# Kernel optimization log

Measured on AMD Instinct MI355X. Metric: run time of the kernel, lower is better.

Reference implementation:

```python
import jax, jax.numpy as jnp
import numpy as np

B, S, H, E, V, NSTEPS = 8, 128, 512, 512, 32000, 8


def setup_inputs() -> dict:
    key = jax.random.key(0)
    ks = jax.random.split(key, 24)

    def lin(k, fi, fo):
        return (jax.random.normal(k, (fi, fo), jnp.float32) / np.sqrt(fi).astype(np.float32))

    return {
        "input_ids": jax.random.randint(ks[0], (B, S), 0, V),
        "tree_ids": jax.random.randint(ks[1], (B, NSTEPS, 3, S), 0, S),
        "emb": jax.random.normal(ks[2], (V, E), jnp.float32) * 0.02,
        "W_ioux": lin(ks[3], E, 3 * H),
        "W_iouh_r": lin(ks[4], H, 3 * H),
        "b_iouh_r": jnp.zeros((3 * H,), jnp.float32),
        "W_iouh_l": lin(ks[5], H, 3 * H),
        "b_iouh_l": jnp.zeros((3 * H,), jnp.float32),
        "W_fx": lin(ks[6], E, H),
        "W_fh0": lin(ks[7], H, H),
        "b_fh0": jnp.zeros((H,), jnp.float32),
        "W_fh1": lin(ks[8], H, H),
        "b_fh1": jnp.zeros((H,), jnp.float32),
        "W_fh2": lin(ks[9], H, H),
        "b_fh2": jnp.zeros((H,), jnp.float32),
        "W_fh3": lin(ks[10], H, H),
        "b_fh3": jnp.zeros((H,), jnp.float32),
    }


def _scatter_rows(vals, idx):
    # out[b, idx[b, j], k] += vals[b, j, k]  (torch scatter_add_ along dim 1)
    return jax.vmap(lambda v, i: jnp.zeros_like(v).at[i].add(v))(vals, idx)


def _gather_rows(vals, idx):
    # out[b, j, k] = vals[b, idx[b, j], k]  (torch gather along dim 1)
    return jnp.take_along_axis(vals, idx[:, :, None], axis=1)


def _masked_scatter(dest, mask_rows, src):
    # Exact torch masked_scatter_ semantics: flatten mask/src, fill True slots
    # with consecutive elements of flattened src.
    m = jnp.broadcast_to(mask_rows[:, :, None], dest.shape).reshape(-1)
    pos = jnp.clip(jnp.cumsum(m) - 1, 0, None)
    out = jnp.where(m, src.reshape(-1)[pos], dest.reshape(-1))
    return out.reshape(dest.shape)


def reference(input_ids, tree_ids, emb, W_ioux, W_iouh_r, b_iouh_r, W_iouh_l,
              b_iouh_l, W_fx, W_fh0, b_fh0, W_fh1, b_fh1, W_fh2, b_fh2,
              W_fh3, b_fh3):
    x = emb[input_ids]                      # [B, S, E]
    Hs = W_fx.shape[1]
    iou_x = x @ W_ioux                      # [B, S, 3H], loop-invariant
    fx_x = x @ W_fx                         # [B, S, H],  loop-invariant
    h0 = jnp.zeros(x.shape[:2] + (Hs,), x.dtype)
    c0 = jnp.zeros_like(h0)
    steps = jnp.transpose(tree_ids, (1, 0, 2, 3))  # [n_steps, B, 3, S]

    def step(carry, t):
        h, c = carry
        idx_d, idx_r, idx_l = t[:, 0], t[:, 1], t[:, 2]
        iou_hr = h @ W_iouh_r + b_iouh_r
        iou_hl = h @ W_iouh_l + b_iouh_l
        # torch scatter_add_ with an index of width H into a 3H buffer only
        # touches the first H channels -- replicate that exactly.
        scat = _scatter_rows(iou_hr[..., :Hs], idx_r) + _scatter_rows(iou_hl[..., :Hs], idx_l)
        iou = iou_x.at[..., :Hs].add(scat)
        i, o, u = jnp.split(iou, 3, axis=-1)
        i, o, u = jax.nn.sigmoid(i), jax.nn.sigmoid(o), jnp.tanh(u)
        # fh0 and fh1 share idx_r, fh2 and fh3 share idx_l -> fold linearly.
        fh_r = h @ (W_fh0 + W_fh1) + (b_fh0 + b_fh1)
        fh_l = h @ (W_fh2 + W_fh3) + (b_fh2 + b_fh3)
        f = jax.nn.sigmoid(_gather_rows(fx_x, idx_d)
                           + _gather_rows(fh_r, idx_r)
                           + _gather_rows(fh_l, idx_l))
        fc = f * c
        c_full = i * u + _scatter_rows(fc, idx_d)
        h_full = o * jnp.tanh(c_full)
        mask = idx_d != 0
        h_new = _masked_scatter(h, mask, h_full)
        c_new = _masked_scatter(c, mask, c_full)
        return (h_new, c_new), None

    (h, c), _ = jax.lax.scan(step, (h0, c0), steps)
    return h
```

## Files before the change

### kernel.cpp

```cpp
#include <hip/hip_runtime.h>
#include <hip/hip_bf16.h>

#define B_ 8
#define S_ 128
#define H_ 512
#define E_ 512
#define NST 8
#define R_ 1024
#define N2 2048
#define KD 512
#define LDA 72
#define NBLK 512
#define GRP 64

typedef __hip_bfloat16 bf16;
typedef __attribute__((ext_vector_type(8))) short v8s;
typedef __attribute__((ext_vector_type(4))) float v4f;
typedef unsigned long long u64;

__device__ __forceinline__ float sigm(float x){ return 1.0f/(1.0f + expf(-x)); }
__device__ __forceinline__ float load_in(const void* p, long long i, int isb){
    return isb ? __bfloat162float(((const bf16*)p)[i]) : ((const float*)p)[i];
}
__device__ __forceinline__ int idx_read(const int* p, int j, int is64){
    return is64 ? p[2*j] : p[j];
}
__device__ __forceinline__ unsigned short f2b(float v){
    bf16 b = __float2bfloat16(v);
    return *(unsigned short*)&b;
}

__device__ __forceinline__ float vload1f(const float* p){
    return __hip_atomic_load(p, __ATOMIC_RELAXED, __HIP_MEMORY_SCOPE_AGENT);
}
__device__ __forceinline__ void vstore1(float* p, float v){
    __hip_atomic_store(p, v, __ATOMIC_RELAXED, __HIP_MEMORY_SCOPE_AGENT);
}
__device__ __forceinline__ void vstore_hb2(unsigned short* p, unsigned short a, unsigned short b){
    unsigned int u = (unsigned)a | ((unsigned)b << 16);
    __hip_atomic_store((unsigned int*)p, u, __ATOMIC_RELAXED, __HIP_MEMORY_SCOPE_AGENT);
}
__device__ __forceinline__ v8s vload16(const unsigned short* p){
    union { u64 u[2]; v8s v; } c;
    c.u[0] = __hip_atomic_load((const u64*)p,     __ATOMIC_RELAXED, __HIP_MEMORY_SCOPE_AGENT);
    c.u[1] = __hip_atomic_load(((const u64*)p)+1, __ATOMIC_RELAXED, __HIP_MEMORY_SCOPE_AGENT);
    return c.v;
}

__device__ __forceinline__ void gsync(int* bar, int gen){
    __syncthreads();
    if (threadIdx.x == 0){
        int g = blockIdx.x >> 6;
        int* ga = bar + 64*(1+g);
        int* gd = bar + 64*(9+g);
        int old = __hip_atomic_fetch_add(ga, 1, __ATOMIC_RELAXED, __HIP_MEMORY_SCOPE_AGENT);
        if (old + 1 == GRP*gen){
            __hip_atomic_fetch_add(bar, GRP, __ATOMIC_RELAXED, __HIP_MEMORY_SCOPE_AGENT);
            while (__hip_atomic_load(bar, __ATOMIC_RELAXED, __HIP_MEMORY_SCOPE_AGENT) < NBLK*gen)
                __builtin_amdgcn_s_sleep(2);
            __hip_atomic_fetch_add(gd, 1, __ATOMIC_RELAXED, __HIP_MEMORY_SCOPE_AGENT);
        } else {
            while (__hip_atomic_load(gd, __ATOMIC_RELAXED, __HIP_MEMORY_SCOPE_AGENT) < gen)
                __builtin_amdgcn_s_sleep(2);
        }
    }
    __syncthreads();
}

__global__ void probe_all(const void* t0, const void* t1, const void* t2, const void* t3,
                          const void* t4, const void* t5, const void* t6, const void* t7,
                          const void* t8, const void* t9, const void* t10, const void* t11,
                          const void* t12, const void* t13, const void* t14,
                          const int* __restrict__ ids, const int* __restrict__ tree,
                          int* __restrict__ flags){
    const void* ts[15] = {t0,t1,t2,t3,t4,t5,t6,t7,t8,t9,t10,t11,t12,t13,t14};
    int bid = blockIdx.x, t = threadIdx.x;
    int bad = 0;
    if (bid < 15){
        if (t < 512){
            unsigned short u = ((const unsigned short*)ts[bid])[t];
            bad = (((u >> 7) & 0xFF) >= 140);
        }
    } else {
        const int* p = (bid == 15) ? ids : tree;
        int n = (bid == 15) ? 1024 : 2048;
        for (int j = t; j < n; j += 1024)
            if (j & 1) bad |= (p[j] != 0);
    }
    unsigned long long bl = __ballot(bad);
    __shared__ int acc[16];
    if ((t & 63) == 0) acc[t >> 6] = (bl != 0ull) ? 1 : 0;
    __syncthreads();
    if (t == 0){
        int any = 0;
        for (int w = 0; w < 16; ++w) any |= acc[w];
        flags[(bid < 15) ? bid : (16 + bid - 15)] = any ? 0 : 1;
    }
}

#define NB2 320
#define GS2 (NB2*512)
__global__ __launch_bounds__(512)
void rank_pack(const void* __restrict__ Wioux, const void* __restrict__ Wfx,
               const void* __restrict__ Wr, const void* __restrict__ Wl,
               const void* __restrict__ W0, const void* __restrict__ W1,
               const void* __restrict__ W2, const void* __restrict__ W3,
               const void* __restrict__ br, const void* __restrict__ bl,
               const void* __restrict__ b0, const void* __restrict__ b1,
               const void* __restrict__ b2, const void* __restrict__ b3,
               const int* __restrict__ ids, const void* __restrict__ emb,
               const int* __restrict__ tree,
               unsigned short* __restrict__ WxT, unsigned short* __restrict__ WcatT,
               float* __restrict__ bcat, unsigned short* __restrict__ xb,
               float* __restrict__ h0,
               int* __restrict__ msk, int* __restrict__ rnk, int* __restrict__ cnt,
               const int* __restrict__ flags, int* __restrict__ bar){
    int bid = blockIdx.x, tid = threadIdx.x;
    int is64 = flags[17];
    if (bid == 0){
        for (int i = tid; i < 64*81; i += 512) bar[i] = 0;
    }
    if (bid < 8){
        int st = bid;
        for (int c = tid; c < R_; c += 512){
            cnt[(0*NST + st)*R_ + c] = 0;
            cnt[(1*NST + st)*R_ + c] = 0;
            cnt[(2*NST + st)*R_ + c] = 0;
        }
        __syncthreads();
        __shared__ int wt[8];
        int runbase = 0;
        for (int ch = 0; ch < 2; ++ch){
            int t = ch*512 + tid;
            int b = t >> 7, s = t & 127;
            int base = (b*NST + st)*3*S_;
            int d0 = idx_read(tree, base + s, is64);
            int rd = (b<<7) + d0;
            int rr = (b<<7) + idx_read(tree, base + S_ + s, is64);
            int rl = (b<<7) + idx_read(tree, base + 2*S_ + s, is64);
            int m = (d0 != 0) ? 1 : 0;
            unsigned long long bal = __ballot(m);
            int lane = tid & 63, wv = tid >> 6;
            if (lane == 0) wt[wv] = __popcll(bal);
            __syncthreads();
            int bp = runbase, tot = 0;
            for (int w = 0; w < wv; ++w) bp += wt[w];
            for (int w = 0; w < 8; ++w) tot += wt[w];
            int rank = bp + __popcll(bal & ((1ull << lane) - 1ull));
            msk[st*R_ + t] = m;
            rnk[st*R_ + t] = m ? rank : 0;
            atomicAdd(&cnt[(0*NST + st)*R_ + rr], 1);
            atomicAdd(&cnt[(1*NST + st)*R_ + rl], 1);
            atomicAdd(&cnt[(2*NST + st)*R_ + rd], 1);
            runbase += tot;
            __syncthreads();
        }
    }
    int gt = bid*512 + tid;
    {
        int f_wx = flags[1], f_wf = flags[6];
        for (int u = gt; u < 131072; u += GS2){
            int n = u >> 6, k0 = (u & 63)*8;
            unsigned short tmp[8];
            #pragma unroll
            for (int i = 0; i < 8; ++i){
                float v = (n < 1536) ? load_in(Wioux, (long long)(k0+i)*1536 + n, f_wx)
                                     : load_in(Wfx,   (long long)(k0+i)*512 + (n-1536), f_wf);
                tmp[i] = f2b(v);
            }
            *(v8s*)&WxT[(size_t)n*KD + k0] = *(v8s*)tmp;
        }
    }
    {
        int fWr=flags[2], fWl=flags[4], fW0=flags[7], fW1=flags[9], fW2=flags[11], fW3=flags[13];
        for (int u = gt; u < 131072; u += GS2){
            int n = u >> 6, k0 = (u & 63)*8;
            unsigned short tmp[8];
            #pragma unroll
            for (int i = 0; i < 8; ++i){
                long long k = k0 + i;
                float v;
                if      (n <  512) v = load_in(Wr, k*1536 + n, fWr);
                else if (n < 1024) v = load_in(Wl, k*1536 + (n-512), fWl);
                else if (n < 1536) { int c = n-1024; v = load_in(W0, k*512+c, fW0) + load_in(W1, k*512+c, fW1); }
                else               { int c = n-1536; v = load_in(W2, k*512+c, fW2) + load_in(W3, k*512+c, fW3); }
                tmp[i] = f2b(v);
            }
            *(v8s*)&WcatT[(size_t)n*KD + k0] = *(v8s*)tmp;
        }
    }
    {
        int fbr=flags[3], fbl=flags[5], fb0=flags[8], fb1=flags[10], fb2=flags[12], fb3=flags[14];
        for (int n = gt; n < 2048; n += GS2){
            float v;
            if      (n <  512) v = load_in(br, n, fbr);
            else if (n < 1024) v = load_in(bl, n-512, fbl);
            else if (n < 1536) v = load_in(b0, n-1024, fb0) + load_in(b1, n-1024, fb1);
            else               v = load_in(b2, n-1536, fb2) + load_in(b3, n-1536, fb3);
            bcat[n] = v;
        }
    }
    {
        int f_emb = flags[0], i64i = flags[16];
        for (int u = gt; u < 65536; u += GS2){
            int r = u >> 6, c0 = (u & 63)*8;
            long long base = (long long)idx_read(ids, r, i64i)*E_ + c0;
            unsigned short tmp[8];
            #pragma unroll
            for (int i = 0; i < 8; ++i) tmp[i] = f2b(load_in(emb, base + i, f_emb));
            *(v8s*)&xb[(size_t)r*KD + c0] = *(v8s*)tmp;
        }
    }
    for (int u = gt; u < 262144; u += GS2)
        ((float4*)h0)[u] = make_float4(0.f,0.f,0.f,0.f);
}

__global__ void csr_scan(const int* __restrict__ cnt, int* __restrict__ off,
                         int* __restrict__ cur){
    int st = blockIdx.x, a = blockIdx.y;
    int t = threadIdx.x;
    int base = (a*NST + st)*R_;
    __shared__ int sh[R_];
    int v = cnt[base + t];
    sh[t] = v;
    __syncthreads();
    for (int d = 1; d < R_; d <<= 1){
        int x = (t >= d) ? sh[t - d] : 0;
        __syncthreads();
        sh[t] += x;
        __syncthreads();
    }
    int excl = sh[t] - v;
    off[base + t] = excl;
    cur[base + t] = excl;
}

__global__ __launch_bounds__(512)
void csr_fill(const int* __restrict__ tree, int* __restrict__ cur,
              int* __restrict__ ent, const int* __restrict__ flags){
    int is64 = flags[17];
    int st = blockIdx.x;
    for (int ch = 0; ch < 2; ++ch){
        int t = ch*512 + threadIdx.x;
        int b = t >> 7, s = t & 127;
        int base = (b*NST + st)*3*S_;
        int rd = (b<<7) + idx_read(tree, base + s, is64);
        int rr = (b<<7) + idx_read(tree, base + S_ + s, is64);
        int rl = (b<<7) + idx_read(tree, base + 2*S_ + s, is64);
        int p0 = atomicAdd(&cur[(0*NST + st)*R_ + rr], 1);
        ent[(0*NST + st)*R_ + p0] = t;
        int p1 = atomicAdd(&cur[(1*NST + st)*R_ + rl], 1);
        ent[(1*NST + st)*R_ + p1] = t;
        int p2 = atomicAdd(&cur[(2*NST + st)*R_ + rd], 1);
        ent[(2*NST + st)*R_ + p2] = t | (rr << 10) | (rl << 20);
    }
}

__device__ __forceinline__ void gemm_phase(const unsigned short* __restrict__ A,
               const unsigned short* __restrict__ BT,
               const float* __restrict__ bias,
               float* __restrict__ C,
               short* __restrict__ SMEM)
{
    int bid = blockIdx.x;
    int bn = (bid & 7)*4 + ((bid >> 3) & 3);
    int bm = bid >> 5;
    int tid = threadIdx.x;
    int lane = tid & 63, wave = tid >> 6;
    int grp = wave >> 2, w4 = wave & 3;
    int wm = w4 & 1, wn = w4 >> 1;
    int lm = lane & 15, quad = lane >> 4;
    short* As = SMEM + grp*(2*64*LDA);
    short* Bs = As + 64*LDA;
    v4f acc[2][2];
    #pragma unroll
    for (int i=0;i<2;++i)
        #pragma unroll
        for (int j=0;j<2;++j) acc[i][j] = (v4f)0.0f;

    int t = tid & 255;
    int srow = t >> 3, sg = (t & 7)*8;
    int kb = grp*256;
    const unsigned short* Ab = A  + (size_t)(bm*64)*KD + kb;
    const unsigned short* Bb = BT + (size_t)(bn*64)*KD + kb;
    v8s pa[4][2], pb[2];
    #pragma unroll
    for (int q=0;q<4;++q)
        #pragma unroll
        for (int j=0;j<2;++j)
            pa[q][j] = vload16(Ab + (size_t)(j*32+srow)*KD + q*64 + sg);
    #pragma unroll
    for (int j=0;j<2;++j)
        pb[j] = *(const v8s*)(Bb + (size_t)(j*32+srow)*KD + sg);
    #pragma unroll
    for (int q = 0; q < 4; ++q){
        #pragma unroll
        for (int j=0;j<2;++j){
            *(v8s*)&As[(j*32+srow)*LDA + sg] = pa[q][j];
            *(v8s*)&Bs[(j*32+srow)*LDA + sg] = pb[j];
        }
        __syncthreads();
        if (q < 3){
            #pragma unroll
            for (int j=0;j<2;++j)
                pb[j] = *(const v8s*)(Bb + (size_t)(j*32+srow)*KD + (q+1)*64 + sg);
        }
        #pragma unroll
        for (int kk = 0; kk < 64; kk += 32){
            v8s af[2], bf[2];
            #pragma unroll
            for (int i=0;i<2;++i){
                af[i] = *(const v8s*)&As[(wm*32 + i*16 + lm)*LDA + kk + quad*8];
                bf[i] = *(const v8s*)&Bs[(wn*32 + i*16 + lm)*LDA + kk + quad*8];
            }
            #pragma unroll
            for (int i=0;i<2;++i)
                #pragma unroll
                for (int j=0;j<2;++j)
                    acc[i][j] = __builtin_amdgcn_mfma_f32_16x16x32_bf16(af[i], bf[j], acc[i][j], 0, 0, 0);
        }
        __syncthreads();
    }
    float* Red = (float*)SMEM;
    if (grp){
        #pragma unroll
        for (int i=0;i<2;++i)
            #pragma unroll
            for (int j=0;j<2;++j)
                #pragma unroll
                for (int rg=0;rg<4;++rg)
                    Red[(wm*32 + i*16 + quad*4 + rg)*64 + (wn*32 + j*16 + lm)] = acc[i][j][rg];
    }
    __syncthreads();
    if (!grp){
        #pragma unroll
        for (int j=0;j<2;++j){
            int n = bn*64 + wn*32 + j*16 + lm;
            float bv = bias ? bias[n] : 0.0f;
            #pragma unroll
            for (int i=0;i<2;++i){
                int m0 = bm*64 + wm*32 + i*16 + quad*4;
                #pragma unroll
                for (int rg = 0; rg < 4; ++rg){
                    float v = acc[i][j][rg] + Red[(wm*32 + i*16 + quad*4 + rg)*64 + (wn*32 + j*16 + lm)] + bv;
                    vstore1(&C[(size_t)(m0+rg)*N2 + n], v);
                }
            }
        }
    }
}

__device__ __forceinline__ void epi_phase(const float* __restrict__ XO,
              const float* __restrict__ T, int tstr,
              const float* __restrict__ hc, const float* __restrict__ cc,
              float* __restrict__ hn, float* __restrict__ cn,
              unsigned short* __restrict__ hb, float* __restrict__ out,
              const int* __restrict__ msk, const int* __restrict__ rnk,
              const int* __restrict__ cnt, const int* __restrict__ off,
              const int* __restrict__ ent, int st, int last, int r0)
{
    int c = threadIdx.x;
    #pragma unroll
    for (int rr2 = 0; rr2 < 2; ++rr2){
        int r = r0 + rr2;
        if (!msk[st*R_ + r]){
            float hv = vload1f(&hc[(size_t)r*H_ + c]);
            if (last){
                out[(size_t)r*H_ + c] = hv;
            } else {
                vstore1(&hn[(size_t)r*H_ + c], hv);
                vstore1(&cn[(size_t)r*H_ + c], vload1f(&cc[(size_t)r*H_ + c]));
                unsigned v16 = f2b(hv);
                unsigned o16 = __shfl_down((int)v16, 1);
                if (!(c & 1)) vstore_hb2(&hb[(size_t)r*KD + c], (unsigned short)v16, (unsigned short)o16);
            }
            continue;
        }
        int j = rnk[st*R_ + r];
        int bR = off[(0*NST+st)*R_ + j], dR = cnt[(0*NST+st)*R_ + j];
        int bL = off[(1*NST+st)*R_ + j], dL = cnt[(1*NST+st)*R_ + j];
        int bD = off[(2*NST+st)*R_ + j], dD = cnt[(2*NST+st)*R_ + j];
        const int* eR = ent + (0*NST+st)*R_ + bR;
        const int* eL = ent + (1*NST+st)*R_ + bL;
        const int* eD = ent + (2*NST+st)*R_ + bD;
        const float* xo = XO + (size_t)j*N2;
        float scv = 0.f;
        {
            int e = 0;
            for (; e + 4 <= dR; e += 4){
                int a0=eR[e], a1=eR[e+1], a2=eR[e+2], a3=eR[e+3];
                float t0 = vload1f(&T[(size_t)a0*tstr + c]);
                float t1 = vload1f(&T[(size_t)a1*tstr + c]);
                float t2 = vload1f(&T[(size_t)a2*tstr + c]);
                float t3 = vload1f(&T[(size_t)a3*tstr + c]);
                scv += (t0 + t1) + (t2 + t3);
            }
            for (; e < dR; ++e) scv += vload1f(&T[(size_t)eR[e]*tstr + c]);
        }
        {
            int e = 0;
            for (; e + 4 <= dL; e += 4){
                int a0=eL[e], a1=eL[e+1], a2=eL[e+2], a3=eL[e+3];
                float t0 = vload1f(&T[(size_t)a0*tstr + 512 + c]);
                float t1 = vload1f(&T[(size_t)a1*tstr + 512 + c]);
                float t2 = vload1f(&T[(size_t)a2*tstr + 512 + c]);
                float t3 = vload1f(&T[(size_t)a3*tstr + 512 + c]);
                scv += (t0 + t1) + (t2 + t3);
            }
            for (; e < dL; ++e) scv += vload1f(&T[(size_t)eL[e]*tstr + 512 + c]);
        }
        float fxv = vload1f(&xo[1536 + c]);
        float csc = 0.f;
        {
            int e = 0;
            for (; e + 2 <= dD; e += 2){
                int p0 = eD[e], p1 = eD[e+1];
                int s0 = p0 & 1023, ra0 = (p0 >> 10) & 1023, rb0 = (p0 >> 20) & 1023;
                int s1 = p1 & 1023, ra1 = (p1 >> 10) & 1023, rb1 = (p1 >> 20) & 1023;
                float ta0 = vload1f(&T[(size_t)ra0*tstr + 1024 + c]);
                float tb0 = vload1f(&T[(size_t)rb0*tstr + 1536 + c]);
                float cv0 = vload1f(&cc[(size_t)s0*H_ + c]);
                float ta1 = vload1f(&T[(size_t)ra1*tstr + 1024 + c]);
                float tb1 = vload1f(&T[(size_t)rb1*tstr + 1536 + c]);
                float cv1 = vload1f(&cc[(size_t)s1*H_ + c]);
                csc += sigm(fxv + ta0 + tb0) * cv0 + sigm(fxv + ta1 + tb1) * cv1;
            }
            for (; e < dD; ++e){
                int pk = eD[e];
                int s  = pk & 1023, ra = (pk >> 10) & 1023, rb = (pk >> 20) & 1023;
                float ta = vload1f(&T[(size_t)ra*tstr + 1024 + c]);
                float tb = vload1f(&T[(size_t)rb*tstr + 1536 + c]);
                float cv = vload1f(&cc[(size_t)s*H_ + c]);
                csc += sigm(fxv + ta + tb) * cv;
            }
        }
        float ig = sigm(vload1f(&xo[c]) + scv);
        float og = sigm(vload1f(&xo[512 + c]));
        float ug = tanhf(vload1f(&xo[1024 + c]));
        float cf = ig*ug + csc;
        float hf = og * tanhf(cf);
        if (last){
            out[(size_t)r*H_ + c] = hf;
        } else {
            vstore1(&hn[(size_t)r*H_ + c], hf);
            vstore1(&cn[(size_t)r*H_ + c], cf);
            unsigned v16 = f2b(hf);
            unsigned o16 = __shfl_down((int)v16, 1);
            if (!(c & 1)) vstore_hb2(&hb[(size_t)r*KD + c], (unsigned short)v16, (unsigned short)o16);
        }
    }
}

__global__ __launch_bounds__(512, 4)
void chain_all(const unsigned short* __restrict__ xb,
               const unsigned short* __restrict__ WxT,
               const unsigned short* __restrict__ WcatT,
               const float* __restrict__ bcat,
               float* __restrict__ XO, float* __restrict__ T,
               float* __restrict__ h0, float* __restrict__ c0,
               float* __restrict__ h1, float* __restrict__ c1,
               unsigned short* __restrict__ hb, float* __restrict__ out,
               const int* __restrict__ msk, const int* __restrict__ rnk,
               const int* __restrict__ cnt, const int* __restrict__ off,
               const int* __restrict__ ent, int* bar)
{
    __shared__ short SMEM[4*64*LDA];
    int bid = blockIdx.x;
    int bG  = bid >> 6;
    int r0  = (bG << 7) + ((bid & 63) << 1);
    int* sc = bar + 64*17;
    int gen = 0;

    auto sig = [&](int st){
        __syncthreads();
        if (threadIdx.x == 0)
            __hip_atomic_fetch_add(sc + 64*(st*8 + bG), 1,
                                   __ATOMIC_RELAXED, __HIP_MEMORY_SCOPE_AGENT);
    };
    auto waitc = [&](int st, int b){
        int* p = sc + 64*(st*8 + b);
        while (__hip_atomic_load(p, __ATOMIC_RELAXED, __HIP_MEMORY_SCOPE_AGENT) < 64)
            __builtin_amdgcn_s_sleep(1);
    };

    gemm_phase(xb, WxT, (const float*)nullptr, XO, SMEM);
    sig(0);
    {
        int m0 = msk[r0], m1 = msk[r0 + 1];
        int jb0 = m0 ? (rnk[r0] >> 7) : bG;
        int jb1 = m1 ? (rnk[r0 + 1] >> 7) : bG;
        if (threadIdx.x == 0){
            waitc(0, jb0);
            if (jb1 != jb0) waitc(0, jb1);
        }
        __syncthreads();
        epi_phase(XO, bcat, 0, h0, c0, h1, c1, hb, out,
                  msk, rnk, cnt, off, ent, 0, 0, r0);
    }
    gsync(bar, ++gen);

    for (int st = 1; st < NST; ++st){
        const float* hcp = (st & 1) ? h1 : h0;
        const float* ccp = (st & 1) ? c1 : c0;
        float* hnp = (st & 1) ? h0 : h1;
        float* cnp = (st & 1) ? c0 : c1;
        gemm_phase(hb, WcatT, bcat, T, SMEM);
        sig(st);
        {
            int m0 = msk[st*R_ + r0], m1 = msk[st*R_ + r0 + 1];
            int jb0 = m0 ? (rnk[st*R_ + r0] >> 7) : bG;
            int jb1 = m1 ? (rnk[st*R_ + r0 + 1] >> 7) : bG;
            if (threadIdx.x == 0){
                waitc(st, bG);
                if (jb0 != bG) waitc(st, jb0);
                if (jb1 != bG && jb1 != jb0) waitc(st, jb1);
            }
            __syncthreads();
            epi_phase(XO, T, N2, hcp, ccp, hnp, cnp, hb, out,
                      msk, rnk, cnt, off, ent, st, (st == NST-1) ? 1 : 0, r0);
        }
        if (st < NST-1) gsync(bar, ++gen);
    }
}

extern "C" void kernel_launch(void* const* d_in, const int* in_sizes, int n_in,
                              void* d_out, int out_size, void* d_ws, size_t ws_size,
                              hipStream_t stream) {
    const int* input_ids = (const int*)d_in[0];
    const int* tree      = (const int*)d_in[1];

    char* wp = (char*)d_ws;
    auto alloc = [&](size_t bytes) -> void* {
        void* q = (void*)wp;
        wp += (bytes + 255) & ~(size_t)255;
        return q;
    };
    float*          XO     = (float*)alloc((size_t)R_*N2*4);
    float*          T      = (float*)alloc((size_t)R_*N2*4);
    float*          h0     = (float*)alloc((size_t)R_*H_*4);
    float*          c0     = (float*)alloc((size_t)R_*H_*4);
    float*          h1     = (float*)alloc((size_t)R_*H_*4);
    float*          c1     = (float*)alloc((size_t)R_*H_*4);
    unsigned short* WxT    = (unsigned short*)alloc((size_t)N2*KD*2);
    unsigned short* WcatT  = (unsigned short*)alloc((size_t)N2*KD*2);
    float*          bcat   = (float*)alloc((size_t)N2*4);
    unsigned short* xb     = (unsigned short*)alloc((size_t)R_*KD*2);
    unsigned short* hb     = (unsigned short*)alloc((size_t)R_*KD*2);
    int*            msk    = (int*)alloc((size_t)NST*R_*4);
    int*            rnk    = (int*)alloc((size_t)NST*R_*4);
    int*            cnt    = (int*)alloc((size_t)3*NST*R_*4);
    int*            off    = (int*)alloc((size_t)3*NST*R_*4);
    int*            cur    = (int*)alloc((size_t)3*NST*R_*4);
    int*            ent    = (int*)alloc((size_t)3*NST*R_*4);
    int*            flags  = (int*)alloc(256);
    int*            bar    = (int*)alloc(32768);
    float*          out    = (float*)d_out;

    hipLaunchKernelGGL(probe_all, dim3(17), dim3(1024), 0, stream,
                       d_in[2], d_in[3], d_in[4], d_in[5], d_in[6], d_in[7], d_in[8],
                       d_in[9], d_in[10], d_in[11], d_in[12], d_in[13], d_in[14],
                       d_in[15], d_in[16], input_ids, tree, flags);
    hipLaunchKernelGGL(rank_pack, dim3(NB2), dim3(512), 0, stream,
                       d_in[3], d_in[8],
                       d_in[4], d_in[6], d_in[9], d_in[11], d_in[13], d_in[15],
                       d_in[5], d_in[7], d_in[10], d_in[12], d_in[14], d_in[16],
                       input_ids, d_in[2], tree,
                       WxT, WcatT, bcat, xb, h0, msk, rnk, cnt, flags, bar);
    hipLaunchKernelGGL(csr_scan, dim3(NST, 3), dim3(1024), 0, stream, cnt, off, cur);
    hipLaunchKernelGGL(csr_fill, dim3(NST), dim3(512), 0, stream, tree, cur, ent, flags);

    hipLaunchKernelGGL(chain_all, dim3(NBLK), dim3(512), 0, stream,
                       xb, WxT, WcatT, bcat, XO, T, h0, c0, h1, c1, hb, out,
                       msk, rnk, cnt, off, ent, bar);
}
```

Baseline: 324.6 us.

## Replace atomic loads with plain loads plus per-XCD cache invalidation at barriers

Device-scope relaxed atomic loads on T, XO, h/c and the GEMM A operand are replaced by ordinary cached loads. Visibility across XCDs is kept by having one block per XCD issue a buffer_inv at each grid barrier, while the other blocks on that XCD wait and do a local invalidate. The fine-grained per-group dependency signalling (sig/waitc) is replaced by full grid barriers, adding one extra barrier after the first GEMM. This trades cheaper vectorised cached loads for a more global synchronisation pattern, and relies on the invalidate protocol being sufficient for correctness.

```diff
diff --git a/kernel.cpp b/kernel.cpp
--- a/kernel.cpp
+++ b/kernel.cpp
@@ -30,9 +30,6 @@
     return *(unsigned short*)&b;
 }
 
-__device__ __forceinline__ float vload1f(const float* p){
-    return __hip_atomic_load(p, __ATOMIC_RELAXED, __HIP_MEMORY_SCOPE_AGENT);
-}
 __device__ __forceinline__ void vstore1(float* p, float v){
     __hip_atomic_store(p, v, __ATOMIC_RELAXED, __HIP_MEMORY_SCOPE_AGENT);
 }
@@ -40,14 +37,14 @@
     unsigned int u = (unsigned)a | ((unsigned)b << 16);
     __hip_atomic_store((unsigned int*)p, u, __ATOMIC_RELAXED, __HIP_MEMORY_SCOPE_AGENT);
 }
-__device__ __forceinline__ v8s vload16(const unsigned short* p){
-    union { u64 u[2]; v8s v; } c;
-    c.u[0] = __hip_atomic_load((const u64*)p,     __ATOMIC_RELAXED, __HIP_MEMORY_SCOPE_AGENT);
-    c.u[1] = __hip_atomic_load(((const u64*)p)+1, __ATOMIC_RELAXED, __HIP_MEMORY_SCOPE_AGENT);
-    return c.v;
-}
-
-__device__ __forceinline__ void gsync(int* bar, int gen){
+
+__device__ __forceinline__ int get_xcd(){
+    int x;
+    asm volatile("s_getreg_b32 %0, hwreg(HW_REG_XCC_ID)" : "=s"(x));
+    return x & 7;
+}
+
+__device__ __forceinline__ void gsync(int* bar, int gen, int inv_gen){
     __syncthreads();
     if (threadIdx.x == 0){
         int g = blockIdx.x >> 6;
@@ -62,6 +59,21 @@
         } else {
             while (__hip_atomic_load(gd, __ATOMIC_RELAXED, __HIP_MEMORY_SCOPE_AGENT) < gen)
                 __builtin_amdgcn_s_sleep(2);
+        }
+        if (inv_gen > 0){
+            int x  = get_xcd();
+            int nx = __hip_atomic_load(bar + 64*(17+x), __ATOMIC_RELAXED, __HIP_MEMORY_SCOPE_AGENT);
+            int* xa = bar + 64*(25+x);
+            int* xr = bar + 64*(33+x);
+            int o2 = __hip_atomic_fetch_add(xa, 1, __ATOMIC_RELAXED, __HIP_MEMORY_SCOPE_AGENT);
+            if (o2 + 1 == nx*inv_gen){
+                asm volatile("buffer_inv sc0 sc1\n\ts_waitcnt vmcnt(0)" ::: "memory");
+                __hip_atomic_store(xr, inv_gen, __ATOMIC_RELAXED, __HIP_MEMORY_SCOPE_AGENT);
+            } else {
+                while (__hip_atomic_load(xr, __ATOMIC_RELAXED, __HIP_MEMORY_SCOPE_AGENT) < inv_gen)
+                    __builtin_amdgcn_s_sleep(1);
+                asm volatile("buffer_inv sc0\n\ts_waitcnt vmcnt(0)" ::: "memory");
+            }
         }
     }
     __syncthreads();
@@ -288,7 +300,7 @@
     for (int q=0;q<4;++q)
         #pragma unroll
         for (int j=0;j<2;++j)
-            pa[q][j] = vload16(Ab + (size_t)(j*32+srow)*KD + q*64 + sg);
+            pa[q][j] = *(const v8s*)(Ab + (size_t)(j*32+srow)*KD + q*64 + sg);
     #pragma unroll
     for (int j=0;j<2;++j)
         pb[j] = *(const v8s*)(Bb + (size_t)(j*32+srow)*KD + sg);
@@ -364,12 +376,12 @@
     for (int rr2 = 0; rr2 < 2; ++rr2){
         int r = r0 + rr2;
         if (!msk[st*R_ + r]){
-            float hv = vload1f(&hc[(size_t)r*H_ + c]);
+            float hv = hc[(size_t)r*H_ + c];
             if (last){
                 out[(size_t)r*H_ + c] = hv;
             } else {
                 vstore1(&hn[(size_t)r*H_ + c], hv);
-                vstore1(&cn[(size_t)r*H_ + c], vload1f(&cc[(size_t)r*H_ + c]));
+                vstore1(&cn[(size_t)r*H_ + c], cc[(size_t)r*H_ + c]);
                 unsigned v16 = f2b(hv);
                 unsigned o16 = __shfl_down((int)v16, 1);
                 if (!(c & 1)) vstore_hb2(&hb[(size_t)r*KD + c], (unsigned short)v16, (unsigned short)o16);
@@ -389,27 +401,27 @@
             int e = 0;
             for (; e + 4 <= dR; e += 4){
                 int a0=eR[e], a1=eR[e+1], a2=eR[e+2], a3=eR[e+3];
-                float t0 = vload1f(&T[(size_t)a0*tstr + c]);
-                float t1 = vload1f(&T[(size_t)a1*tstr + c]);
-                float t2 = vload1f(&T[(size_t)a2*tstr + c]);
-                float t3 = vload1f(&T[(size_t)a3*tstr + c]);
+                float t0 = T[(size_t)a0*tstr + c];
+                float t1 = T[(size_t)a1*tstr + c];
+                float t2 = T[(size_t)a2*tstr + c];
+                float t3 = T[(size_t)a3*tstr + c];
                 scv += (t0 + t1) + (t2 + t3);
             }
-            for (; e < dR; ++e) scv += vload1f(&T[(size_t)eR[e]*tstr + c]);
+            for (; e < dR; ++e) scv += T[(size_t)eR[e]*tstr + c];
         }
         {
             int e = 0;
             for (; e + 4 <= dL; e += 4){
                 int a0=eL[e], a1=eL[e+1], a2=eL[e+2], a3=eL[e+3];
-                float t0 = vload1f(&T[(size_t)a0*tstr + 512 + c]);
-                float t1 = vload1f(&T[(size_t)a1*tstr + 512 + c]);
-                float t2 = vload1f(&T[(size_t)a2*tstr + 512 + c]);
-                float t3 = vload1f(&T[(size_t)a3*tstr + 512 + c]);
+                float t0 = T[(size_t)a0*tstr + 512 + c];
+                float t1 = T[(size_t)a1*tstr + 512 + c];
+                float t2 = T[(size_t)a2*tstr + 512 + c];
+                float t3 = T[(size_t)a3*tstr + 512 + c];
                 scv += (t0 + t1) + (t2 + t3);
             }
-            for (; e < dL; ++e) scv += vload1f(&T[(size_t)eL[e]*tstr + 512 + c]);
-        }
-        float fxv = vload1f(&xo[1536 + c]);
+            for (; e < dL; ++e) scv += T[(size_t)eL[e]*tstr + 512 + c];
+        }
+        float fxv = xo[1536 + c];
         float csc = 0.f;
         {
             int e = 0;
@@ -417,26 +429,26 @@
                 int p0 = eD[e], p1 = eD[e+1];
                 int s0 = p0 & 1023, ra0 = (p0 >> 10) & 1023, rb0 = (p0 >> 20) & 1023;
                 int s1 = p1 & 1023, ra1 = (p1 >> 10) & 1023, rb1 = (p1 >> 20) & 1023;
-                float ta0 = vload1f(&T[(size_t)ra0*tstr + 1024 + c]);
-                float tb0 = vload1f(&T[(size_t)rb0*tstr + 1536 + c]);
-                float cv0 = vload1f(&cc[(size_t)s0*H_ + c]);
-                float ta1 = vload1f(&T[(size_t)ra1*tstr + 1024 + c]);
-                float tb1 = vload1f(&T[(size_t)rb1*tstr + 1536 + c]);
-                float cv1 = vload1f(&cc[(size_t)s1*H_ + c]);
+                float ta0 = T[(size_t)ra0*tstr + 1024 + c];
+                float tb0 = T[(size_t)rb0*tstr + 1536 + c];
+                float cv0 = cc[(size_t)s0*H_ + c];
+                float ta1 = T[(size_t)ra1*tstr + 1024 + c];
+                float tb1 = T[(size_t)rb1*tstr + 1536 + c];
+                float cv1 = cc[(size_t)s1*H_ + c];
                 csc += sigm(fxv + ta0 + tb0) * cv0 + sigm(fxv + ta1 + tb1) * cv1;
             }
             for (; e < dD; ++e){
                 int pk = eD[e];
                 int s  = pk & 1023, ra = (pk >> 10) & 1023, rb = (pk >> 20) & 1023;
-                float ta = vload1f(&T[(size_t)ra*tstr + 1024 + c]);
-                float tb = vload1f(&T[(size_t)rb*tstr + 1536 + c]);
-                float cv = vload1f(&cc[(size_t)s*H_ + c]);
+                float ta = T[(size_t)ra*tstr + 1024 + c];
+                float tb = T[(size_t)rb*tstr + 1536 + c];
+                float cv = cc[(size_t)s*H_ + c];
                 csc += sigm(fxv + ta + tb) * cv;
             }
         }
-        float ig = sigm(vload1f(&xo[c]) + scv);
-        float og = sigm(vload1f(&xo[512 + c]));
-        float ug = tanhf(vload1f(&xo[1024 + c]));
+        float ig = sigm(xo[c] + scv);
+        float og = sigm(xo[512 + c]);
+        float ug = tanhf(xo[1024 + c]);
         float cf = ig*ug + csc;
         float hf = og * tanhf(cf);
         if (last){
@@ -465,39 +477,17 @@
                const int* __restrict__ ent, int* bar)
 {
     __shared__ short SMEM[4*64*LDA];
-    int bid = blockIdx.x;
-    int bG  = bid >> 6;
-    int r0  = (bG << 7) + ((bid & 63) << 1);
-    int* sc = bar + 64*17;
-    int gen = 0;
-
-    auto sig = [&](int st){
-        __syncthreads();
-        if (threadIdx.x == 0)
-            __hip_atomic_fetch_add(sc + 64*(st*8 + bG), 1,
-                                   __ATOMIC_RELAXED, __HIP_MEMORY_SCOPE_AGENT);
-    };
-    auto waitc = [&](int st, int b){
-        int* p = sc + 64*(st*8 + b);
-        while (__hip_atomic_load(p, __ATOMIC_RELAXED, __HIP_MEMORY_SCOPE_AGENT) < 64)
-            __builtin_amdgcn_s_sleep(1);
-    };
+    if (threadIdx.x == 0){
+        int x = get_xcd();
+        __hip_atomic_fetch_add(bar + 64*(17+x), 1, __ATOMIC_RELAXED, __HIP_MEMORY_SCOPE_AGENT);
+    }
+    int r0 = blockIdx.x*2;
+    int gen = 0, ig = 0;
 
     gemm_phase(xb, WxT, (const float*)nullptr, XO, SMEM);
-    sig(0);
-    {
-        int m0 = msk[r0], m1 = msk[r0 + 1];
-        int jb0 = m0 ? (rnk[r0] >> 7) : bG;
-        int jb1 = m1 ? (rnk[r0 + 1] >> 7) : bG;
-        if (threadIdx.x == 0){
-            waitc(0, jb0);
-            if (jb1 != jb0) waitc(0, jb1);
-        }
-        __syncthreads();
-        epi_phase(XO, bcat, 0, h0, c0, h1, c1, hb, out,
-                  msk, rnk, cnt, off, ent, 0, 0, r0);
-    }
-    gsync(bar, ++gen);
+    gsync(bar, ++gen, 0);
+    epi_phase(XO, bcat, 0, h0, c0, h1, c1, hb, out, msk, rnk, cnt, off, ent, 0, 0, r0);
+    gsync(bar, ++gen, 0);
 
     for (int st = 1; st < NST; ++st){
         const float* hcp = (st & 1) ? h1 : h0;
@@ -505,21 +495,10 @@
         float* hnp = (st & 1) ? h0 : h1;
         float* cnp = (st & 1) ? c0 : c1;
         gemm_phase(hb, WcatT, bcat, T, SMEM);
-        sig(st);
-        {
-            int m0 = msk[st*R_ + r0], m1 = msk[st*R_ + r0 + 1];
-            int jb0 = m0 ? (rnk[st*R_ + r0] >> 7) : bG;
-            int jb1 = m1 ? (rnk[st*R_ + r0 + 1] >> 7) : bG;
-            if (threadIdx.x == 0){
-                waitc(st, bG);
-                if (jb0 != bG) waitc(st, jb0);
-                if (jb1 != bG && jb1 != jb0) waitc(st, jb1);
-            }
-            __syncthreads();
-            epi_phase(XO, T, N2, hcp, ccp, hnp, cnp, hb, out,
-                      msk, rnk, cnt, off, ent, st, (st == NST-1) ? 1 : 0, r0);
-        }
-        if (st < NST-1) gsync(bar, ++gen);
+        gsync(bar, ++gen, (st >= 2) ? ++ig : 0);
+        epi_phase(XO, T, N2, hcp, ccp, hnp, cnp, hb, out,
+                  msk, rnk, cnt, off, ent, st, (st == NST-1) ? 1 : 0, r0);
+        if (st < NST-1) gsync(bar, ++gen, ++ig);
     }
 }
 
```

Result: no change. 329.3 us (+1.4%).
